# Kernel tuning notes

Measured on AMD Instinct MI355X. Metric: run time of the kernel, lower is better.

The kernel has to match this reference:

```python
import jax, jax.numpy as jnp
import numpy as np

N_NODES = 50000
N_EDGES = 1600000
NEG_SLOPE = 0.2


def _gat_layer(x, src, dst, W, a_src, a_dst, b, n_nodes):
    # PyG GATConv (heads=1, concat=True): h = xW; e_ij = LeakyReLU(a_src.h_j + a_dst.h_i)
    # alpha = softmax over incoming edges of each target i; out_i = sum_j alpha_ij h_j + b
    h = x @ W                                   # [N, out]
    alpha_src = h @ a_src                        # [N]
    alpha_dst = h @ a_dst                        # [N]
    e = alpha_src[src] + alpha_dst[dst]          # [E]
    e = jnp.where(e > 0, e, NEG_SLOPE * e)       # leaky_relu(0.2)
    m = jax.ops.segment_max(e, dst, num_segments=n_nodes)   # per-target max
    ex = jnp.exp(e - m[dst])
    denom = jax.ops.segment_sum(ex, dst, num_segments=n_nodes)
    alpha = ex / (denom[dst] + 1e-16)            # [E]
    out = jax.ops.segment_sum(alpha[:, None] * h[src], dst, num_segments=n_nodes)
    return out + b


def setup_inputs() -> dict:
    key = jax.random.key(0)
    ks = jax.random.split(key, 16)
    hid, out_dim, in_dim = 128, 5, 13
    x = jax.random.normal(ks[0], (N_NODES, in_dim), dtype=jnp.float32)
    edge_index = jax.random.randint(ks[1], (2, N_EDGES), 0, N_NODES, dtype=jnp.int64)
    s = 0.1
    return {
        "x": x,
        "edge_index": edge_index,
        "W1": jax.random.normal(ks[2], (in_dim, hid), dtype=jnp.float32) * s,
        "a_src1": jax.random.normal(ks[3], (hid,), dtype=jnp.float32) * s,
        "a_dst1": jax.random.normal(ks[4], (hid,), dtype=jnp.float32) * s,
        "b1": jnp.zeros((hid,), dtype=jnp.float32),
        "W2": jax.random.normal(ks[5], (hid, hid), dtype=jnp.float32) * s,
        "a_src2": jax.random.normal(ks[6], (hid,), dtype=jnp.float32) * s,
        "a_dst2": jax.random.normal(ks[7], (hid,), dtype=jnp.float32) * s,
        "b2": jnp.zeros((hid,), dtype=jnp.float32),
        "W3": jax.random.normal(ks[8], (hid, out_dim), dtype=jnp.float32) * s,
        "a_src3": jax.random.normal(ks[9], (out_dim,), dtype=jnp.float32) * s,
        "a_dst3": jax.random.normal(ks[10], (out_dim,), dtype=jnp.float32) * s,
        "b3": jnp.zeros((out_dim,), dtype=jnp.float32),
    }


def reference(x, edge_index, W1, a_src1, a_dst1, b1, W2, a_src2, a_dst2, b2,
              W3, a_src3, a_dst3, b3):
    n = x.shape[0]
    # GATConv add_self_loops=True: append (i, i) edges
    loops = jnp.arange(n, dtype=edge_index.dtype)
    src = jnp.concatenate([edge_index[0], loops])
    dst = jnp.concatenate([edge_index[1], loops])
    h = _gat_layer(x, src, dst, W1, a_src1, a_dst1, b1, n)
    h = jax.nn.relu(h)  # dropout identity in eval mode
    h = _gat_layer(h, src, dst, W2, a_src2, a_dst2, b2, n)
    h = jax.nn.relu(h)
    h = _gat_layer(h, src, dst, W3, a_src3, a_dst3, b3, n)
    return jax.nn.log_softmax(h, axis=1)
```

## Files before the change

kernel.cpp:

```cpp
#include <hip/hip_runtime.h>
#include <hip/hip_bf16.h>


#define LEAKY(e) ((e) > 0.f ? (e) : 0.2f * (e))
__device__ inline float clamp30(float e) { return fminf(fmaxf(e, -30.f), 30.f); }
__device__ inline float expc(float e) { return __expf(clamp30(LEAKY(e))); }

__device__ inline float ldany(const void* p, int bf, int i) {
    return bf ? __bfloat162float(((const __hip_bfloat16*)p)[i])
              : ((const float*)p)[i];
}
__device__ inline int ldidx(const void* p, int i64, long long i) {
    return i64 ? (int)(((const unsigned int*)p)[2 * i])
               : ((const int*)p)[i];
}

__device__ inline float bflo(unsigned int w) { return __uint_as_float(w << 16); }
__device__ inline float bfhi(unsigned int w) { return __uint_as_float(w & 0xffff0000u); }
__device__ inline unsigned int packbf(float a, float b) {
    __hip_bfloat16 x = __float2bfloat16(a), y = __float2bfloat16(b);
    unsigned short ux, uy;
    __builtin_memcpy(&ux, &x, 2); __builtin_memcpy(&uy, &y, 2);
    return (unsigned int)ux | ((unsigned int)uy << 16);
}

__global__ void detect_kernel(const void* W1, const void* ei, int* flags) {
    if (threadIdx.x == 0 && blockIdx.x == 0) {
        const unsigned int* w = (const unsigned int*)W1;
        int c = 0;
        for (int i = 0; i < 64; i++) {
            unsigned int e = (w[i] >> 7) & 0xFFu;
            if (e >= 0x70u && e <= 0x7Fu) c++;
        }
        flags[0] = (c >= 32) ? 1 : 0;
        const unsigned int* q = (const unsigned int*)ei;
        int z = 0;
        for (int i = 0; i < 64; i++)
            if (q[2 * i + 1] == 0u) z++;
        flags[1] = (z >= 32) ? 1 : 0;
    }
}


__global__ __launch_bounds__(256) void sortA_hist(
    const void* __restrict__ ei, const int* __restrict__ flags,
    int* __restrict__ blockHist, int E, int NBUK)
{
    __shared__ int hist[512];
    const int i64 = flags[1];
    const int tid = threadIdx.x, blk = blockIdx.x;
    for (int i = tid; i < NBUK; i += 256) hist[i] = 0;
    __syncthreads();
    const int chunk = (E + 255) / 256;
    const int e0 = blk * chunk, e1 = min(e0 + chunk, E);
    for (int t = e0 + tid; t < e1; t += 256) {
        int d = ldidx(ei, i64, (long long)E + t);
        atomicAdd(&hist[d >> 7], 1);
    }
    __syncthreads();
    for (int i = tid; i < NBUK; i += 256)
        blockHist[blk * NBUK + i] = hist[i];
}

__global__ __launch_bounds__(256) void sortB_prefix(
    int* __restrict__ blockHist, int* __restrict__ bucketBase, int NBUK)
{
    __shared__ int wt[4];
    __shared__ int wbase[4];
    const int b = blockIdx.x;
    const int tid = threadIdx.x, lane = tid & 63, wid = tid >> 6;
    int v = blockHist[tid * NBUK + b];
    int x = v;
#pragma unroll
    for (int o = 1; o < 64; o <<= 1) {
        int y = __shfl_up(x, o);
        if (lane >= o) x += y;
    }
    if (lane == 63) wt[wid] = x;
    __syncthreads();
    if (tid == 0) {
        int s = 0;
#pragma unroll
        for (int i = 0; i < 4; i++) { wbase[i] = s; s += wt[i]; }
        bucketBase[b] = s;
    }
    __syncthreads();
    blockHist[tid * NBUK + b] = x - v + wbase[wid];
}

__global__ __launch_bounds__(512) void sortB2_scan(
    int* __restrict__ bucketBase, int NBUK)
{
    __shared__ int wt[8];
    __shared__ int wbase[8];
    __shared__ int total_s;
    const int tid = threadIdx.x, lane = tid & 63, wid = tid >> 6;
    int v = (tid < NBUK) ? bucketBase[tid] : 0;
    int x = v;
#pragma unroll
    for (int o = 1; o < 64; o <<= 1) {
        int y = __shfl_up(x, o);
        if (lane >= o) x += y;
    }
    if (lane == 63) wt[wid] = x;
    __syncthreads();
    if (tid == 0) {
        int s = 0;
#pragma unroll
        for (int i = 0; i < 8; i++) { wbase[i] = s; s += wt[i]; }
        total_s = s;
    }
    __syncthreads();
    if (tid < NBUK) bucketBase[tid] = x - v + wbase[wid];
    if (tid == 0) bucketBase[NBUK] = total_s;
}

__global__ __launch_bounds__(256) void sortC_scatter(
    const void* __restrict__ ei, const int* __restrict__ flags,
    const int* __restrict__ blockHist, const int* __restrict__ bucketBase,
    unsigned int* __restrict__ pairbuf, int E, int NBUK)
{
    __shared__ int cur[512];
    const int i64 = flags[1];
    const int tid = threadIdx.x, blk = blockIdx.x;
    for (int i = tid; i < NBUK; i += 256)
        cur[i] = blockHist[blk * NBUK + i] + bucketBase[i];
    __syncthreads();
    const int chunk = (E + 255) / 256;
    const int e0 = blk * chunk, e1 = min(e0 + chunk, E);
    for (int t = e0 + tid; t < e1; t += 256) {
        int s = ldidx(ei, i64, t);
        int d = ldidx(ei, i64, (long long)E + t);
        int pos = atomicAdd(&cur[d >> 7], 1);
        pairbuf[pos] = ((unsigned int)(d & 127) << 16) | (unsigned int)s;
    }
}

__global__ __launch_bounds__(256) void sortD_bin(
    const unsigned int* __restrict__ pairbuf, const int* __restrict__ bucketBase,
    int* __restrict__ rowptr, int* __restrict__ ssrc, int N, int NBUK, int E)
{
    __shared__ int cnt[128];
    __shared__ int cur2[128];
    __shared__ int wt1;
    const int b = blockIdx.x;
    const int tid = threadIdx.x, lane = tid & 63;
    const int e0 = bucketBase[b], e1 = bucketBase[b + 1];
    if (tid < 128) cnt[tid] = 0;
    __syncthreads();
    for (int i = e0 + tid; i < e1; i += 256)
        atomicAdd(&cnt[pairbuf[i] >> 16], 1);
    __syncthreads();
    if (tid < 128) {
        int v = cnt[tid];
        int x = v;
#pragma unroll
        for (int o = 1; o < 64; o <<= 1) {
            int y = __shfl_up(x, o);
            if (lane >= o) x += y;
        }
        if (tid == 63) wt1 = x;
        __syncthreads();
        if (tid >= 64) x += wt1;
        int pfx = x - v;
        cur2[tid] = pfx;
        int node = b * 128 + tid;
        if (node < N) rowptr[node] = e0 + pfx;
    } else {
        __syncthreads();
    }
    if (b == NBUK - 1 && tid == 0) rowptr[N] = e1;
    __syncthreads();
    for (int i = e0 + tid; i < e1; i += 256) {
        unsigned int w = pairbuf[i];
        int p = atomicAdd(&cur2[w >> 16], 1);
        ssrc[e0 + p] = (int)(w & 0xFFFFu);
    }
}


__global__ __launch_bounds__(256) void node_prep13(
    const void* __restrict__ xin, const void* __restrict__ Wg,
    const void* __restrict__ asg, const void* __restrict__ adg,
    const int* __restrict__ flags,
    unsigned int* __restrict__ h2, float* __restrict__ asrc,
    float* __restrict__ adst, int N)
{
    const int bf = flags[0];
    __shared__ float Wlds[13 * 128];
    for (int i = threadIdx.x; i < 13 * 128; i += 256)
        Wlds[i] = ldany(Wg, bf, i);
    __syncthreads();
    const int lane = threadIdx.x & 63;
    int wave = (blockIdx.x * 256 + threadIdx.x) >> 6;
    int nw = (gridDim.x * 256) >> 6;
    float a0 = ldany(asg, bf, 2 * lane), a1 = ldany(asg, bf, 2 * lane + 1);
    float d0 = ldany(adg, bf, 2 * lane), d1 = ldany(adg, bf, 2 * lane + 1);
    for (int n = wave; n < N; n += nw) {
        float x0 = (lane < 13) ? ldany(xin, bf, n * 13 + lane) : 0.f;
        float s0 = 0.f, s1 = 0.f;
#pragma unroll
        for (int k = 0; k < 13; k++) {
            float xv = __shfl(x0, k);
            s0 += xv * Wlds[k * 128 + 2 * lane];
            s1 += xv * Wlds[k * 128 + 2 * lane + 1];
        }
        float pa = s0 * a0 + s1 * a1;
        float pd = s0 * d0 + s1 * d1;
#pragma unroll
        for (int o = 32; o > 0; o >>= 1) {
            pa += __shfl_xor(pa, o);
            pd += __shfl_xor(pd, o);
        }
        if (lane == 0) { asrc[n] = pa; adst[n] = pd; }
        h2[(size_t)n * 64 + lane] = packbf(s0, s1);
    }
}

__global__ __launch_bounds__(256) void gemm128(
    const float* __restrict__ X, const void* __restrict__ Wg,
    const void* __restrict__ asg, const void* __restrict__ adg,
    const int* __restrict__ flags, unsigned int* __restrict__ h2,
    float* __restrict__ asrc, float* __restrict__ adst, int N)
{
    const int bf = flags[0];
    __shared__ float Ws[32 * 132];
    __shared__ float xT[32 * 132];
    const int tid = threadIdx.x;
    const int ox = tid & 15;
    const int ny = tid >> 4;
    const int nb0 = blockIdx.x * 128;

    float acc[8][8];
#pragma unroll
    for (int i = 0; i < 8; i++)
#pragma unroll
        for (int j = 0; j < 8; j++) acc[i][j] = 0.f;

    for (int kc = 0; kc < 128; kc += 32) {
        if (!bf) {
            const float4* Wg4 = (const float4*)((const float*)Wg + kc * 128);
#pragma unroll
            for (int it = 0; it < 4; it++) {
                int f = it * 256 + tid;
                float4 v = Wg4[f];
                *(float4*)&Ws[(f >> 5) * 132 + (f & 31) * 4] = v;
            }
        } else {
            for (int i = tid; i < 32 * 128; i += 256)
                Ws[(i >> 7) * 132 + (i & 127)] = ldany(Wg, 1, kc * 128 + i);
        }
#pragma unroll
        for (int it = 0; it < 4; it++) {
            int f = it * 256 + tid;
            int n = f >> 3, kq = f & 7;
            int node = min(nb0 + n, N - 1);
            float4 v = *(const float4*)&X[(size_t)node * 128 + kc + kq * 4];
            xT[(kq * 4 + 0) * 132 + n] = v.x;
            xT[(kq * 4 + 1) * 132 + n] = v.y;
            xT[(kq * 4 + 2) * 132 + n] = v.z;
            xT[(kq * 4 + 3) * 132 + n] = v.w;
        }
        __syncthreads();
#pragma unroll 4
        for (int k = 0; k < 32; k++) {
            float4 w0 = *(float4*)&Ws[k * 132 + 8 * ox];
            float4 w1 = *(float4*)&Ws[k * 132 + 8 * ox + 4];
            float4 x0 = *(float4*)&xT[k * 132 + 8 * ny];
            float4 x1 = *(float4*)&xT[k * 132 + 8 * ny + 4];
            float xv[8] = {x0.x, x0.y, x0.z, x0.w, x1.x, x1.y, x1.z, x1.w};
            float wv[8] = {w0.x, w0.y, w0.z, w0.w, w1.x, w1.y, w1.z, w1.w};
#pragma unroll
            for (int i = 0; i < 8; i++)
#pragma unroll
                for (int j = 0; j < 8; j++) acc[i][j] += xv[i] * wv[j];
        }
        __syncthreads();
    }
    float as_[8], ad_[8];
#pragma unroll
    for (int j = 0; j < 8; j++) {
        as_[j] = ldany(asg, bf, 8 * ox + j);
        ad_[j] = ldany(adg, bf, 8 * ox + j);
    }
#pragma unroll
    for (int i = 0; i < 8; i++) {
        int node = nb0 + 8 * ny + i;
        float pa = 0.f, pd = 0.f;
#pragma unroll
        for (int j = 0; j < 8; j++) {
            pa += acc[i][j] * as_[j];
            pd += acc[i][j] * ad_[j];
        }
#pragma unroll
        for (int o = 1; o < 16; o <<= 1) {
            pa += __shfl_xor(pa, o);
            pd += __shfl_xor(pd, o);
        }
        if (node < N) {
            if (ox == 0) { asrc[node] = pa; adst[node] = pd; }
            unsigned int p0 = packbf(acc[i][0], acc[i][1]);
            unsigned int p1 = packbf(acc[i][2], acc[i][3]);
            unsigned int p2 = packbf(acc[i][4], acc[i][5]);
            unsigned int p3 = packbf(acc[i][6], acc[i][7]);
            uint4 pv = {p0, p1, p2, p3};
            *(uint4*)&h2[(size_t)node * 64 + 4 * ox] = pv;
        }
    }
}

__global__ __launch_bounds__(256) void proj7(
    const float* __restrict__ X, const void* __restrict__ W3,
    const void* __restrict__ as3, const void* __restrict__ ad3,
    const int* __restrict__ flags, float* __restrict__ h3,
    float* __restrict__ asrc, float* __restrict__ adst, int N)
{
    const int bf = flags[0];
    __shared__ float Wp[128 * 8];
    __shared__ float xs[256 * 33];
    const int tid = threadIdx.x;
    for (int i = tid; i < 128 * 8; i += 256) {
        int k = i >> 3, j = i & 7;
        float v = 0.f;
        if (j < 5) v = ldany(W3, bf, k * 5 + j);
        else if (j == 5) v = ldany(as3, bf, k);
        else if (j == 6) v = ldany(ad3, bf, k);
        Wp[i] = v;
    }
    const int nb0 = blockIdx.x * 256;
    float acc[7] = {0.f, 0.f, 0.f, 0.f, 0.f, 0.f, 0.f};
    for (int kc = 0; kc < 128; kc += 32) {
        __syncthreads();
#pragma unroll
        for (int it = 0; it < 32; it++) {
            int f = it * 256 + tid;
            int row = f >> 5, k = f & 31;
            int node = nb0 + row;
            xs[row * 33 + k] = (node < N) ? X[(size_t)node * 128 + kc + k] : 0.f;
        }
        __syncthreads();
#pragma unroll
        for (int k = 0; k < 32; k++) {
            float xv = xs[tid * 33 + k];
            float4 w0 = *(float4*)&Wp[(kc + k) * 8];
            float4 w1 = *(float4*)&Wp[(kc + k) * 8 + 4];
            acc[0] += xv * w0.x; acc[1] += xv * w0.y; acc[2] += xv * w0.z;
            acc[3] += xv * w0.w; acc[4] += xv * w1.x; acc[5] += xv * w1.y;
            acc[6] += xv * w1.z;
        }
    }
    int node = nb0 + tid;
    if (node < N) {
        h3[(size_t)node * 5 + 0] = acc[0];
        h3[(size_t)node * 5 + 1] = acc[1];
        h3[(size_t)node * 5 + 2] = acc[2];
        h3[(size_t)node * 5 + 3] = acc[3];
        h3[(size_t)node * 5 + 4] = acc[4];
        asrc[node] = acc[5];
        adst[node] = acc[6];
    }
}


__device__ inline int rdl(int v, int j) { return __builtin_amdgcn_readlane(v, j); }
__device__ inline float rdlf(float v, int j) {
    return __uint_as_float((unsigned int)__builtin_amdgcn_readlane((int)__float_as_uint(v), j));
}

__global__ __launch_bounds__(256) void agg_fused128(
    const int* __restrict__ rowptr, const int* __restrict__ ssrc,
    const unsigned int* __restrict__ h2, const float* __restrict__ asrc,
    const float* __restrict__ adst, const void* __restrict__ bias,
    const int* __restrict__ flags, float* __restrict__ feat, int N)
{
    const int bf = flags[0];
    const int lane = threadIdx.x & 63;
    int wave = (blockIdx.x * 256 + threadIdx.x) >> 6;
    int nw = (gridDim.x * 256) >> 6;
    const float bx = ldany(bias, bf, 2 * lane);
    const float by = ldany(bias, bf, 2 * lane + 1);

    for (int n = wave; n < N; n += nw) {
        float ad = adst[n];
        float wself = expc(asrc[n] + ad);
        unsigned int hw = h2[(size_t)n * 64 + lane];
        float accx = wself * bflo(hw), accy = wself * bfhi(hw);
        float wpart = (lane == 0) ? wself : 0.f;
        const int start = rowptr[n], end = rowptr[n + 1];
        for (int base = start; base < end; base += 64) {
            int sl = 0;
            float wl = 0.f;
            if (base + lane < end) {
                sl = ssrc[base + lane];
                wl = expc(asrc[sl] + ad);
            }
            wpart += wl;
            const int cnt = min(64, end - base);
            int j = 0;
            for (; j + 8 <= cnt; j += 8) {
                int s0 = rdl(sl, j + 0), s1 = rdl(sl, j + 1);
                int s2 = rdl(sl, j + 2), s3 = rdl(sl, j + 3);
                int s4 = rdl(sl, j + 4), s5 = rdl(sl, j + 5);
                int s6 = rdl(sl, j + 6), s7 = rdl(sl, j + 7);
                unsigned int u0 = h2[(size_t)s0 * 64 + lane];
                unsigned int u1 = h2[(size_t)s1 * 64 + lane];
                unsigned int u2 = h2[(size_t)s2 * 64 + lane];
                unsigned int u3 = h2[(size_t)s3 * 64 + lane];
                unsigned int u4 = h2[(size_t)s4 * 64 + lane];
                unsigned int u5 = h2[(size_t)s5 * 64 + lane];
                unsigned int u6 = h2[(size_t)s6 * 64 + lane];
                unsigned int u7 = h2[(size_t)s7 * 64 + lane];
                float w0 = rdlf(wl, j + 0), w1 = rdlf(wl, j + 1);
                float w2 = rdlf(wl, j + 2), w3 = rdlf(wl, j + 3);
                float w4 = rdlf(wl, j + 4), w5 = rdlf(wl, j + 5);
                float w6 = rdlf(wl, j + 6), w7 = rdlf(wl, j + 7);
                accx += w0 * bflo(u0); accy += w0 * bfhi(u0);
                accx += w1 * bflo(u1); accy += w1 * bfhi(u1);
                accx += w2 * bflo(u2); accy += w2 * bfhi(u2);
                accx += w3 * bflo(u3); accy += w3 * bfhi(u3);
                accx += w4 * bflo(u4); accy += w4 * bfhi(u4);
                accx += w5 * bflo(u5); accy += w5 * bfhi(u5);
                accx += w6 * bflo(u6); accy += w6 * bfhi(u6);
                accx += w7 * bflo(u7); accy += w7 * bfhi(u7);
            }
            for (; j < cnt; j++) {
                int s = rdl(sl, j);
                float w = rdlf(wl, j);
                unsigned int ww = h2[(size_t)s * 64 + lane];
                accx += w * bflo(ww);
                accy += w * bfhi(ww);
            }
        }
        float wsum = wpart;
#pragma unroll
        for (int o = 32; o > 0; o >>= 1) wsum += __shfl_xor(wsum, o);
        float inv = 1.f / (wsum + 1e-16f);
        float2 ov = {fmaxf(accx * inv + bx, 0.f), fmaxf(accy * inv + by, 0.f)};
        *(float2*)&feat[(size_t)n * 128 + 2 * lane] = ov;
    }
}

__global__ __launch_bounds__(256) void agg_fused5(
    const int* __restrict__ rowptr, const int* __restrict__ ssrc,
    const float* __restrict__ h3, const float* __restrict__ asrc,
    const float* __restrict__ adst, const void* __restrict__ b3,
    const int* __restrict__ flags, float* __restrict__ out, int N)
{
    const int bf = flags[0];
    const int lane = threadIdx.x & 63;
    int wave = (blockIdx.x * 256 + threadIdx.x) >> 6;
    int nw = (gridDim.x * 256) >> 6;

    for (int n = wave; n < N; n += nw) {
        float ad = adst[n];
        float a0 = 0.f, a1 = 0.f, a2 = 0.f, a3 = 0.f, a4 = 0.f, wsum = 0.f;
        if (lane == 0) {
            float w = expc(asrc[n] + ad);
            wsum = w;
            a0 = w * h3[n * 5 + 0]; a1 = w * h3[n * 5 + 1]; a2 = w * h3[n * 5 + 2];
            a3 = w * h3[n * 5 + 3]; a4 = w * h3[n * 5 + 4];
        }
        const int start = rowptr[n], end = rowptr[n + 1];
        for (int i = start + lane; i < end; i += 64) {
            int s = ssrc[i];
            float w = expc(asrc[s] + ad);
            wsum += w;
            a0 += w * h3[s * 5 + 0]; a1 += w * h3[s * 5 + 1]; a2 += w * h3[s * 5 + 2];
            a3 += w * h3[s * 5 + 3]; a4 += w * h3[s * 5 + 4];
        }
#pragma unroll
        for (int o = 32; o > 0; o >>= 1) {
            a0 += __shfl_xor(a0, o); a1 += __shfl_xor(a1, o); a2 += __shfl_xor(a2, o);
            a3 += __shfl_xor(a3, o); a4 += __shfl_xor(a4, o); wsum += __shfl_xor(wsum, o);
        }
        if (lane == 0) {
            float inv = 1.f / (wsum + 1e-16f);
            float v0 = a0 * inv + ldany(b3, bf, 0);
            float v1 = a1 * inv + ldany(b3, bf, 1);
            float v2 = a2 * inv + ldany(b3, bf, 2);
            float v3 = a3 * inv + ldany(b3, bf, 3);
            float v4 = a4 * inv + ldany(b3, bf, 4);
            float m = fmaxf(fmaxf(fmaxf(v0, v1), fmaxf(v2, v3)), v4);
            float s = __expf(v0 - m) + __expf(v1 - m) + __expf(v2 - m)
                    + __expf(v3 - m) + __expf(v4 - m);
            float lse = m + __logf(s);
            out[n * 5 + 0] = v0 - lse; out[n * 5 + 1] = v1 - lse;
            out[n * 5 + 2] = v2 - lse; out[n * 5 + 3] = v3 - lse;
            out[n * 5 + 4] = v4 - lse;
        }
    }
}

extern "C" void kernel_launch(void* const* d_in, const int* in_sizes, int n_in,
                              void* d_out, int out_size, void* d_ws, size_t ws_size,
                              hipStream_t stream)
{
    const void* x  = d_in[0];
    const void* ei = d_in[1];
    const void* W1 = d_in[2];
    const void* as1= d_in[3];
    const void* ad1= d_in[4];
    const void* b1 = d_in[5];
    const void* W2 = d_in[6];
    const void* as2= d_in[7];
    const void* ad2= d_in[8];
    const void* b2 = d_in[9];
    const void* W3 = d_in[10];
    const void* as3= d_in[11];
    const void* ad3= d_in[12];
    const void* b3 = d_in[13];

    const int N = in_sizes[0] / 13;
    const int E = in_sizes[1] / 2;
    const int NBUK = (N + 127) / 128;

    float* ws    = (float*)d_ws;
    float* feat  = ws;
    unsigned int* h2 = (unsigned int*)(feat + (size_t)N * 128);
    float* asrc  = (float*)(h2 + (size_t)N * 64);
    float* adst  = asrc + N;
    float* h3    = adst + N;
    int*   rowptr= (int*)(h3 + (size_t)N * 5);
    int*   bucketBase = rowptr + N + 1;
    int*   blockHist  = bucketBase + NBUK + 1;
    unsigned int* pairbuf = (unsigned int*)(blockHist + 256 * NBUK);
    int*   ssrc  = (int*)(pairbuf + E);
    int*   flags = ssrc + E;

    const int wb = (N + 3) / 4;
    const int gb = (N + 127) / 128;
    const int pb = (N + 255) / 256;

    detect_kernel<<<1, 64, 0, stream>>>(W1, ei, flags);

    sortA_hist<<<256, 256, 0, stream>>>(ei, flags, blockHist, E, NBUK);
    sortB_prefix<<<NBUK, 256, 0, stream>>>(blockHist, bucketBase, NBUK);
    sortB2_scan<<<1, 512, 0, stream>>>(bucketBase, NBUK);
    sortC_scatter<<<256, 256, 0, stream>>>(ei, flags, blockHist, bucketBase,
                                           pairbuf, E, NBUK);
    sortD_bin<<<NBUK, 256, 0, stream>>>(pairbuf, bucketBase, rowptr, ssrc,
                                        N, NBUK, E);

    node_prep13<<<1024, 256, 0, stream>>>(x, W1, as1, ad1, flags, h2, asrc, adst, N);
    agg_fused128<<<wb, 256, 0, stream>>>(rowptr, ssrc, h2, asrc, adst, b1, flags, feat, N);

    gemm128<<<gb, 256, 0, stream>>>(feat, W2, as2, ad2, flags, h2, asrc, adst, N);
    agg_fused128<<<wb, 256, 0, stream>>>(rowptr, ssrc, h2, asrc, adst, b2, flags, feat, N);

    proj7<<<pb, 256, 0, stream>>>(feat, W3, as3, ad3, flags, h3, asrc, adst, N);
    agg_fused5<<<wb, 256, 0, stream>>>(rowptr, ssrc, h3, asrc, adst, b3, flags,
                                       (float*)d_out, N);
}
```

Before: 355.7 us.

## Use bf16 MFMA for layer-2 GEMM, single-pass bucket scatter, 16-bit source indices

```diff
diff --git a/kernel.cpp b/kernel.cpp
--- a/kernel.cpp
+++ b/kernel.cpp
@@ -3,6 +3,7 @@
 
 
 #define LEAKY(e) ((e) > 0.f ? (e) : 0.2f * (e))
+#define CAPB 6144
 __device__ inline float clamp30(float e) { return fminf(fmaxf(e, -30.f), 30.f); }
 __device__ inline float expc(float e) { return __expf(clamp30(LEAKY(e))); }
 
@@ -17,12 +18,16 @@
 
 __device__ inline float bflo(unsigned int w) { return __uint_as_float(w << 16); }
 __device__ inline float bfhi(unsigned int w) { return __uint_as_float(w & 0xffff0000u); }
+__device__ inline unsigned short bfbits(float a) {
+    __hip_bfloat16 x = __float2bfloat16(a);
+    unsigned short u; __builtin_memcpy(&u, &x, 2); return u;
+}
 __device__ inline unsigned int packbf(float a, float b) {
-    __hip_bfloat16 x = __float2bfloat16(a), y = __float2bfloat16(b);
-    unsigned short ux, uy;
-    __builtin_memcpy(&ux, &x, 2); __builtin_memcpy(&uy, &y, 2);
-    return (unsigned int)ux | ((unsigned int)uy << 16);
-}
+    return (unsigned int)bfbits(a) | ((unsigned int)bfbits(b) << 16);
+}
+
+typedef __attribute__((ext_vector_type(8))) short short8;
+typedef __attribute__((ext_vector_type(4))) float f32x4;
 
 __global__ void detect_kernel(const void* W1, const void* ei, int* flags) {
     if (threadIdx.x == 0 && blockIdx.x == 0) {
@@ -42,60 +47,57 @@
 }
 
 
-__global__ __launch_bounds__(256) void sortA_hist(
+__global__ __launch_bounds__(256) void zero_ints(int* p, int n) {
+    int i = blockIdx.x * 256 + threadIdx.x;
+    if (i < n) p[i] = 0;
+}
+
+__global__ __launch_bounds__(256) void scatter1(
     const void* __restrict__ ei, const int* __restrict__ flags,
-    int* __restrict__ blockHist, int E, int NBUK)
-{
+    int* __restrict__ gcur, unsigned int* __restrict__ pairbuf, int E, int NBUK)
+{
+    __shared__ unsigned int ebuf[6400];
     __shared__ int hist[512];
+    __shared__ int wbase[512];
     const int i64 = flags[1];
     const int tid = threadIdx.x, blk = blockIdx.x;
-    for (int i = tid; i < NBUK; i += 256) hist[i] = 0;
-    __syncthreads();
     const int chunk = (E + 255) / 256;
     const int e0 = blk * chunk, e1 = min(e0 + chunk, E);
-    for (int t = e0 + tid; t < e1; t += 256) {
-        int d = ldidx(ei, i64, (long long)E + t);
-        atomicAdd(&hist[d >> 7], 1);
-    }
-    __syncthreads();
-    for (int i = tid; i < NBUK; i += 256)
-        blockHist[blk * NBUK + i] = hist[i];
-}
-
-__global__ __launch_bounds__(256) void sortB_prefix(
-    int* __restrict__ blockHist, int* __restrict__ bucketBase, int NBUK)
-{
-    __shared__ int wt[4];
-    __shared__ int wbase[4];
-    const int b = blockIdx.x;
-    const int tid = threadIdx.x, lane = tid & 63, wid = tid >> 6;
-    int v = blockHist[tid * NBUK + b];
-    int x = v;
-#pragma unroll
-    for (int o = 1; o < 64; o <<= 1) {
-        int y = __shfl_up(x, o);
-        if (lane >= o) x += y;
-    }
-    if (lane == 63) wt[wid] = x;
-    __syncthreads();
-    if (tid == 0) {
-        int s = 0;
-#pragma unroll
-        for (int i = 0; i < 4; i++) { wbase[i] = s; s += wt[i]; }
-        bucketBase[b] = s;
-    }
-    __syncthreads();
-    blockHist[tid * NBUK + b] = x - v + wbase[wid];
+    for (int sub = e0; sub < e1; sub += 6400) {
+        const int cnt = min(6400, e1 - sub);
+        for (int i = tid; i < NBUK; i += 256) hist[i] = 0;
+        __syncthreads();
+        for (int i = tid; i < cnt; i += 256) {
+            int s = ldidx(ei, i64, sub + i);
+            int d = ldidx(ei, i64, (long long)E + sub + i);
+            ebuf[i] = ((unsigned int)d << 16) | (unsigned int)s;
+            atomicAdd(&hist[d >> 7], 1);
+        }
+        __syncthreads();
+        for (int b = tid; b < NBUK; b += 256) {
+            int h = hist[b];
+            wbase[b] = (h > 0) ? (b * CAPB + atomicAdd(&gcur[b], h)) : 0;
+            hist[b] = 0;
+        }
+        __syncthreads();
+        for (int i = tid; i < cnt; i += 256) {
+            unsigned int w = ebuf[i];
+            int b = (int)(w >> 23);
+            int p = atomicAdd(&hist[b], 1);
+            pairbuf[wbase[b] + p] = w;
+        }
+        __syncthreads();
+    }
 }
 
 __global__ __launch_bounds__(512) void sortB2_scan(
-    int* __restrict__ bucketBase, int NBUK)
+    const int* __restrict__ gcur, int* __restrict__ bucketBase, int NBUK)
 {
     __shared__ int wt[8];
     __shared__ int wbase[8];
     __shared__ int total_s;
     const int tid = threadIdx.x, lane = tid & 63, wid = tid >> 6;
-    int v = (tid < NBUK) ? bucketBase[tid] : 0;
+    int v = (tid < NBUK) ? gcur[tid] : 0;
     int x = v;
 #pragma unroll
     for (int o = 1; o < 64; o <<= 1) {
@@ -115,30 +117,10 @@
     if (tid == 0) bucketBase[NBUK] = total_s;
 }
 
-__global__ __launch_bounds__(256) void sortC_scatter(
-    const void* __restrict__ ei, const int* __restrict__ flags,
-    const int* __restrict__ blockHist, const int* __restrict__ bucketBase,
-    unsigned int* __restrict__ pairbuf, int E, int NBUK)
-{
-    __shared__ int cur[512];
-    const int i64 = flags[1];
-    const int tid = threadIdx.x, blk = blockIdx.x;
-    for (int i = tid; i < NBUK; i += 256)
-        cur[i] = blockHist[blk * NBUK + i] + bucketBase[i];
-    __syncthreads();
-    const int chunk = (E + 255) / 256;
-    const int e0 = blk * chunk, e1 = min(e0 + chunk, E);
-    for (int t = e0 + tid; t < e1; t += 256) {
-        int s = ldidx(ei, i64, t);
-        int d = ldidx(ei, i64, (long long)E + t);
-        int pos = atomicAdd(&cur[d >> 7], 1);
-        pairbuf[pos] = ((unsigned int)(d & 127) << 16) | (unsigned int)s;
-    }
-}
-
 __global__ __launch_bounds__(256) void sortD_bin(
     const unsigned int* __restrict__ pairbuf, const int* __restrict__ bucketBase,
-    int* __restrict__ rowptr, int* __restrict__ ssrc, int N, int NBUK, int E)
+    int* __restrict__ rowptr, unsigned short* __restrict__ ssrc,
+    int N, int NBUK)
 {
     __shared__ int cnt[128];
     __shared__ int cur2[128];
@@ -146,10 +128,12 @@
     const int b = blockIdx.x;
     const int tid = threadIdx.x, lane = tid & 63;
     const int e0 = bucketBase[b], e1 = bucketBase[b + 1];
+    const int nloc = e1 - e0;
+    const unsigned int* pb = pairbuf + (size_t)b * CAPB;
     if (tid < 128) cnt[tid] = 0;
     __syncthreads();
-    for (int i = e0 + tid; i < e1; i += 256)
-        atomicAdd(&cnt[pairbuf[i] >> 16], 1);
+    for (int i = tid; i < nloc; i += 256)
+        atomicAdd(&cnt[(pb[i] >> 16) & 127], 1);
     __syncthreads();
     if (tid < 128) {
         int v = cnt[tid];
@@ -171,10 +155,10 @@
     }
     if (b == NBUK - 1 && tid == 0) rowptr[N] = e1;
     __syncthreads();
-    for (int i = e0 + tid; i < e1; i += 256) {
-        unsigned int w = pairbuf[i];
-        int p = atomicAdd(&cur2[w >> 16], 1);
-        ssrc[e0 + p] = (int)(w & 0xFFFFu);
+    for (int i = tid; i < nloc; i += 256) {
+        unsigned int w = pb[i];
+        int p = atomicAdd(&cur2[(w >> 16) & 127], 1);
+        ssrc[e0 + p] = (unsigned short)(w & 0xFFFFu);
     }
 }
 
@@ -217,95 +201,90 @@
     }
 }
 
-__global__ __launch_bounds__(256) void gemm128(
+__global__ __launch_bounds__(256) void gemm_mfma(
     const float* __restrict__ X, const void* __restrict__ Wg,
     const void* __restrict__ asg, const void* __restrict__ adg,
     const int* __restrict__ flags, unsigned int* __restrict__ h2,
     float* __restrict__ asrc, float* __restrict__ adst, int N)
 {
     const int bf = flags[0];
-    __shared__ float Ws[32 * 132];
-    __shared__ float xT[32 * 132];
+    __shared__ unsigned short A_s[64 * 136];
+    __shared__ unsigned short B_s[128 * 136];
     const int tid = threadIdx.x;
-    const int ox = tid & 15;
-    const int ny = tid >> 4;
-    const int nb0 = blockIdx.x * 128;
-
-    float acc[8][8];
-#pragma unroll
-    for (int i = 0; i < 8; i++)
-#pragma unroll
-        for (int j = 0; j < 8; j++) acc[i][j] = 0.f;
-
-    for (int kc = 0; kc < 128; kc += 32) {
+    const int nb0 = blockIdx.x * 64;
+
+#pragma unroll
+    for (int it = 0; it < 16; it++) {
+        int f = it * 256 + tid;
+        int k = f >> 5, ng = (f & 31) * 4;
         if (!bf) {
-            const float4* Wg4 = (const float4*)((const float*)Wg + kc * 128);
-#pragma unroll
-            for (int it = 0; it < 4; it++) {
-                int f = it * 256 + tid;
-                float4 v = Wg4[f];
-                *(float4*)&Ws[(f >> 5) * 132 + (f & 31) * 4] = v;
-            }
+            float4 v = *(const float4*)((const float*)Wg + k * 128 + ng);
+            B_s[(ng + 0) * 136 + k] = bfbits(v.x);
+            B_s[(ng + 1) * 136 + k] = bfbits(v.y);
+            B_s[(ng + 2) * 136 + k] = bfbits(v.z);
+            B_s[(ng + 3) * 136 + k] = bfbits(v.w);
         } else {
-            for (int i = tid; i < 32 * 128; i += 256)
-                Ws[(i >> 7) * 132 + (i & 127)] = ldany(Wg, 1, kc * 128 + i);
-        }
-#pragma unroll
-        for (int it = 0; it < 4; it++) {
-            int f = it * 256 + tid;
-            int n = f >> 3, kq = f & 7;
-            int node = min(nb0 + n, N - 1);
-            float4 v = *(const float4*)&X[(size_t)node * 128 + kc + kq * 4];
-            xT[(kq * 4 + 0) * 132 + n] = v.x;
-            xT[(kq * 4 + 1) * 132 + n] = v.y;
-            xT[(kq * 4 + 2) * 132 + n] = v.z;
-            xT[(kq * 4 + 3) * 132 + n] = v.w;
-        }
-        __syncthreads();
-#pragma unroll 4
-        for (int k = 0; k < 32; k++) {
-            float4 w0 = *(float4*)&Ws[k * 132 + 8 * ox];
-            float4 w1 = *(float4*)&Ws[k * 132 + 8 * ox + 4];
-            float4 x0 = *(float4*)&xT[k * 132 + 8 * ny];
-            float4 x1 = *(float4*)&xT[k * 132 + 8 * ny + 4];
-            float xv[8] = {x0.x, x0.y, x0.z, x0.w, x1.x, x1.y, x1.z, x1.w};
-            float wv[8] = {w0.x, w0.y, w0.z, w0.w, w1.x, w1.y, w1.z, w1.w};
-#pragma unroll
-            for (int i = 0; i < 8; i++)
-#pragma unroll
-                for (int j = 0; j < 8; j++) acc[i][j] += xv[i] * wv[j];
-        }
-        __syncthreads();
-    }
-    float as_[8], ad_[8];
-#pragma unroll
-    for (int j = 0; j < 8; j++) {
-        as_[j] = ldany(asg, bf, 8 * ox + j);
-        ad_[j] = ldany(adg, bf, 8 * ox + j);
-    }
-#pragma unroll
-    for (int i = 0; i < 8; i++) {
-        int node = nb0 + 8 * ny + i;
+            const unsigned short* W16 = (const unsigned short*)Wg;
+            B_s[(ng + 0) * 136 + k] = W16[k * 128 + ng + 0];
+            B_s[(ng + 1) * 136 + k] = W16[k * 128 + ng + 1];
+            B_s[(ng + 2) * 136 + k] = W16[k * 128 + ng + 2];
+            B_s[(ng + 3) * 136 + k] = W16[k * 128 + ng + 3];
+        }
+    }
+#pragma unroll
+    for (int it = 0; it < 8; it++) {
+        int f = it * 256 + tid;
+        int n = f >> 5, g = f & 31;
+        int node = min(nb0 + n, N - 1);
+        float4 v = *(const float4*)&X[(size_t)node * 128 + g * 4];
+        unsigned int* dst = (unsigned int*)&A_s[n * 136 + g * 4];
+        dst[0] = packbf(v.x, v.y);
+        dst[1] = packbf(v.z, v.w);
+    }
+    __syncthreads();
+
+    const int wv = tid >> 6;
+    const int lane = tid & 63;
+    const int m = lane & 15, quad = lane >> 4;
+
+    f32x4 acc[8];
+#pragma unroll
+    for (int c = 0; c < 8; c++) acc[c] = (f32x4){0.f, 0.f, 0.f, 0.f};
+
+#pragma unroll
+    for (int q = 0; q < 4; q++) {
+        short8 a = *(const short8*)&A_s[(wv * 16 + m) * 136 + q * 32 + quad * 8];
+#pragma unroll
+        for (int c = 0; c < 8; c++) {
+            short8 b = *(const short8*)&B_s[(c * 16 + m) * 136 + q * 32 + quad * 8];
+            acc[c] = __builtin_amdgcn_mfma_f32_16x16x32_bf16(a, b, acc[c], 0, 0, 0);
+        }
+    }
+
+    float asv[8], adv[8];
+#pragma unroll
+    for (int c = 0; c < 8; c++) {
+        asv[c] = ldany(asg, bf, c * 16 + m);
+        adv[c] = ldany(adg, bf, c * 16 + m);
+    }
+    unsigned short* h2u = (unsigned short*)h2;
+#pragma unroll
+    for (int reg = 0; reg < 4; reg++) {
+        int node = nb0 + wv * 16 + quad * 4 + reg;
         float pa = 0.f, pd = 0.f;
 #pragma unroll
-        for (int j = 0; j < 8; j++) {
-            pa += acc[i][j] * as_[j];
-            pd += acc[i][j] * ad_[j];
+        for (int c = 0; c < 8; c++) {
+            float v = acc[c][reg];
+            pa += v * asv[c];
+            pd += v * adv[c];
+            if (node < N) h2u[(size_t)node * 128 + c * 16 + m] = bfbits(v);
         }
 #pragma unroll
         for (int o = 1; o < 16; o <<= 1) {
             pa += __shfl_xor(pa, o);
             pd += __shfl_xor(pd, o);
         }
-        if (node < N) {
-            if (ox == 0) { asrc[node] = pa; adst[node] = pd; }
-            unsigned int p0 = packbf(acc[i][0], acc[i][1]);
-            unsigned int p1 = packbf(acc[i][2], acc[i][3]);
-            unsigned int p2 = packbf(acc[i][4], acc[i][5]);
-            unsigned int p3 = packbf(acc[i][6], acc[i][7]);
-            uint4 pv = {p0, p1, p2, p3};
-            *(uint4*)&h2[(size_t)node * 64 + 4 * ox] = pv;
-        }
+        if (node < N && m == 0) { asrc[node] = pa; adst[node] = pd; }
     }
 }
 
@@ -368,7 +347,7 @@
 }
 
 __global__ __launch_bounds__(256) void agg_fused128(
-    const int* __restrict__ rowptr, const int* __restrict__ ssrc,
+    const int* __restrict__ rowptr, const unsigned short* __restrict__ ssrc,
     const unsigned int* __restrict__ h2, const float* __restrict__ asrc,
     const float* __restrict__ adst, const void* __restrict__ bias,
     const int* __restrict__ flags, float* __restrict__ feat, int N)
@@ -391,7 +370,7 @@
             int sl = 0;
             float wl = 0.f;
             if (base + lane < end) {
-                sl = ssrc[base + lane];
+                sl = (int)ssrc[base + lane];
                 wl = expc(asrc[sl] + ad);
             }
             wpart += wl;
@@ -441,7 +420,7 @@
 }
 
 __global__ __launch_bounds__(256) void agg_fused5(
-    const int* __restrict__ rowptr, const int* __restrict__ ssrc,
+    const int* __restrict__ rowptr, const unsigned short* __restrict__ ssrc,
     const float* __restrict__ h3, const float* __restrict__ asrc,
     const float* __restrict__ adst, const void* __restrict__ b3,
     const int* __restrict__ flags, float* __restrict__ out, int N)
@@ -462,7 +441,7 @@
         }
         const int start = rowptr[n], end = rowptr[n + 1];
         for (int i = start + lane; i < end; i += 64) {
-            int s = ssrc[i];
+            int s = (int)ssrc[i];
             float w = expc(asrc[s] + ad);
             wsum += w;
             a0 += w * h3[s * 5 + 0]; a1 += w * h3[s * 5 + 1]; a2 += w * h3[s * 5 + 2];
@@ -522,32 +501,29 @@
     float* h3    = adst + N;
     int*   rowptr= (int*)(h3 + (size_t)N * 5);
     int*   bucketBase = rowptr + N + 1;
-    int*   blockHist  = bucketBase + NBUK + 1;
-    unsigned int* pairbuf = (unsigned int*)(blockHist + 256 * NBUK);
-    int*   ssrc  = (int*)(pairbuf + E);
-    int*   flags = ssrc + E;
+    int*   gcur  = bucketBase + NBUK + 1;
+    unsigned int* pairbuf = (unsigned int*)(gcur + NBUK);
+    unsigned short* ssrc16 = (unsigned short*)(pairbuf + (size_t)NBUK * CAPB);
+    int*   flags = (int*)(ssrc16 + E);
 
     const int wb = (N + 3) / 4;
-    const int gb = (N + 127) / 128;
+    const int gb = (N + 63) / 64;
     const int pb = (N + 255) / 256;
 
     detect_kernel<<<1, 64, 0, stream>>>(W1, ei, flags);
 
-    sortA_hist<<<256, 256, 0, stream>>>(ei, flags, blockHist, E, NBUK);
-    sortB_prefix<<<NBUK, 256, 0, stream>>>(blockHist, bucketBase, NBUK);
-    sortB2_scan<<<1, 512, 0, stream>>>(bucketBase, NBUK);
-    sortC_scatter<<<256, 256, 0, stream>>>(ei, flags, blockHist, bucketBase,
-                                           pairbuf, E, NBUK);
-    sortD_bin<<<NBUK, 256, 0, stream>>>(pairbuf, bucketBase, rowptr, ssrc,
-                                        N, NBUK, E);
+    zero_ints<<<(NBUK + 255) / 256, 256, 0, stream>>>(gcur, NBUK);
+    scatter1<<<256, 256, 0, stream>>>(ei, flags, gcur, pairbuf, E, NBUK);
+    sortB2_scan<<<1, 512, 0, stream>>>(gcur, bucketBase, NBUK);
+    sortD_bin<<<NBUK, 256, 0, stream>>>(pairbuf, bucketBase, rowptr, ssrc16, N, NBUK);
 
     node_prep13<<<1024, 256, 0, stream>>>(x, W1, as1, ad1, flags, h2, asrc, adst, N);
-    agg_fused128<<<wb, 256, 0, stream>>>(rowptr, ssrc, h2, asrc, adst, b1, flags, feat, N);
-
-    gemm128<<<gb, 256, 0, stream>>>(feat, W2, as2, ad2, flags, h2, asrc, adst, N);
-    agg_fused128<<<wb, 256, 0, stream>>>(rowptr, ssrc, h2, asrc, adst, b2, flags, feat, N);
+    agg_fused128<<<wb, 256, 0, stream>>>(rowptr, ssrc16, h2, asrc, adst, b1, flags, feat, N);
+
+    gemm_mfma<<<gb, 256, 0, stream>>>(feat, W2, as2, ad2, flags, h2, asrc, adst, N);
+    agg_fused128<<<wb, 256, 0, stream>>>(rowptr, ssrc16, h2, asrc, adst, b2, flags, feat, N);
 
     proj7<<<pb, 256, 0, stream>>>(feat, W3, as3, ad3, flags, h3, asrc, adst, N);
-    agg_fused5<<<wb, 256, 0, stream>>>(rowptr, ssrc, h3, asrc, adst, b3, flags,
+    agg_fused5<<<wb, 256, 0, stream>>>(rowptr, ssrc16, h3, asrc, adst, b3, flags,
                                        (float*)d_out, N);
 }
```

After: 343.6 us. -3.4%, faster.
